# Kernel tuning notes

Measured on AMD Instinct MI355X. Metric: run time of the kernel, lower is better.

The kernel has to match this reference:

```python
import jax, jax.numpy as jnp
import numpy as np

B, N, D, H, DH, L, DFF, NSP = 2048, 64, 256, 8, 32, 3, 1024, 120
SCALE = 0.05


def _layernorm(x, g, b, eps=1e-5):
    m = x.mean(-1, keepdims=True)
    v = ((x - m) ** 2).mean(-1, keepdims=True)
    return (x - m) * jax.lax.rsqrt(v + eps) * g + b


def forward_core(input_messages, momenta, edge_vectors, edge_distances, cutoff_factors,
                 edge_w, edge_b, node_table, mom_w, mom_b, node_comp_w, node_comp_b,
                 nbr_table, comp_w1, comp_b1, comp_w2, comp_b2,
                 qkv_w, qkv_b, attn_out_w, attn_out_b, ln1_g, ln1_b,
                 ffn_w1, ffn_b1, ffn_w2, ffn_b2, ln2_g, ln2_b,
                 padding_mask, element_indices_nodes, element_indices_neighbors):
    silu = jax.nn.silu
    # NodeEncoder: element embedding + momenta projection, compressed to d_model
    node = node_table[element_indices_nodes]                       # [B, D]
    mom = momenta @ mom_w + mom_b                                  # [B, D]
    node = jnp.concatenate([node, mom], -1) @ node_comp_w + node_comp_b  # [B, D]
    # edge embedding: [vec(3), dist(1)] -> Linear(4, D)
    edge = jnp.concatenate([edge_vectors, edge_distances[..., None]], -1) @ edge_w + edge_b  # [B,N,D]
    # merge edge / neighbor-element / incoming message embeddings, compress MLP
    tok = jnp.concatenate([edge, nbr_table[element_indices_neighbors], input_messages], -1)  # [B,N,3D]
    tok = silu(tok @ comp_w1 + comp_b1) @ comp_w2 + comp_b2        # [B,N,D]
    x = jnp.concatenate([node[:, None, :], tok], 1)                # [B,S,D], S=N+1
    # cutoff factors: prepend 1 for central token, zero padded tokens, apply as log-bias over keys
    ones_col = jnp.ones((x.shape[0], 1), x.dtype)
    cf = jnp.concatenate([ones_col, cutoff_factors], 1)            # [B,S]
    mask = jnp.concatenate([jnp.ones((x.shape[0], 1), bool), padding_mask], 1)
    cf = jnp.where(mask, cf, jnp.zeros((), x.dtype))
    bias = jnp.where(cf > 0, jnp.log(jnp.maximum(cf, 1e-30)), jnp.full((), -1e9, x.dtype))
    bias = bias[:, None, None, :]                                  # [B,1,1,S] (key dim)
    Bsz, S, _ = x.shape
    inv_sqrt_dh = 1.0 / np.sqrt(DH).astype(np.float32)
    for l in range(L):  # PostLN transformer layers
        qkv = (x @ qkv_w[l] + qkv_b[l]).reshape(Bsz, S, 3, H, DH)
        q, k, v = qkv[:, :, 0], qkv[:, :, 1], qkv[:, :, 2]         # [B,S,H,DH]
        scores = jnp.einsum('bqhd,bkhd->bhqk', q, k) * inv_sqrt_dh + bias
        a = jax.nn.softmax(scores, axis=-1)                        # cutoff-modulated attention
        o = jnp.einsum('bhqk,bkhd->bqhd', a, v).reshape(Bsz, S, D)
        x = _layernorm(x + (o @ attn_out_w[l] + attn_out_b[l]), ln1_g[l], ln1_b[l])
        h = silu(x @ ffn_w1[l] + ffn_b1[l]) @ ffn_w2[l] + ffn_b2[l]
        x = _layernorm(x + h, ln2_g[l], ln2_b[l])
    return x


def setup_inputs() -> dict:
    key = jax.random.key(0)
    ks = iter(jax.random.split(key, 48))
    def nrm(shape, s=SCALE):
        return jax.random.normal(next(ks), shape, dtype=jnp.float32) * s
    inp = {
        'input_messages': jax.random.normal(next(ks), (B, N, D), dtype=jnp.float32),
        'momenta': jax.random.normal(next(ks), (B, 3), dtype=jnp.float32),
        'edge_vectors': jax.random.normal(next(ks), (B, N, 3), dtype=jnp.float32),
        'edge_distances': jax.random.uniform(next(ks), (B, N), dtype=jnp.float32) * 5.0,
        'cutoff_factors': jax.random.uniform(next(ks), (B, N), dtype=jnp.float32),
        'padding_mask': jnp.ones((B, N), dtype=bool),
        'element_indices_nodes': jax.random.randint(next(ks), (B,), 0, NSP),
        'element_indices_neighbors': jax.random.randint(next(ks), (B, N), 0, NSP),
        'edge_w': nrm((4, D)), 'edge_b': jnp.zeros((D,), jnp.float32),
        'node_table': nrm((NSP, D), 1.0), 'mom_w': nrm((3, D)), 'mom_b': jnp.zeros((D,), jnp.float32),
        'node_comp_w': nrm((2 * D, D)), 'node_comp_b': jnp.zeros((D,), jnp.float32),
        'nbr_table': nrm((NSP, D), 1.0),
        'comp_w1': nrm((3 * D, D)), 'comp_b1': jnp.zeros((D,), jnp.float32),
        'comp_w2': nrm((D, D)), 'comp_b2': jnp.zeros((D,), jnp.float32),
        'qkv_w': nrm((L, D, 3 * D)), 'qkv_b': jnp.zeros((L, 3 * D), jnp.float32),
        'attn_out_w': nrm((L, D, D)), 'attn_out_b': jnp.zeros((L, D), jnp.float32),
        'ln1_g': jnp.ones((L, D), jnp.float32), 'ln1_b': jnp.zeros((L, D), jnp.float32),
        'ffn_w1': nrm((L, D, DFF)), 'ffn_b1': jnp.zeros((L, DFF), jnp.float32),
        'ffn_w2': nrm((L, DFF, D)), 'ffn_b2': jnp.zeros((L, D), jnp.float32),
        'ln2_g': jnp.ones((L, D), jnp.float32), 'ln2_b': jnp.zeros((L, D), jnp.float32),
        'use_manual_attention': 1,
    }
    return inp


def reference(input_messages, momenta, edge_vectors, edge_distances, cutoff_factors,
              padding_mask, element_indices_nodes, element_indices_neighbors,
              edge_w, edge_b, node_table, mom_w, mom_b, node_comp_w, node_comp_b,
              nbr_table, comp_w1, comp_b1, comp_w2, comp_b2,
              qkv_w, qkv_b, attn_out_w, attn_out_b, ln1_g, ln1_b,
              ffn_w1, ffn_b1, ffn_w2, ffn_b2, ln2_g, ln2_b, use_manual_attention):
    # use_manual_attention selects an implementation path in torch; math is identical.
    x = forward_core(input_messages, momenta, edge_vectors, edge_distances, cutoff_factors,
                     edge_w, edge_b, node_table, mom_w, mom_b, node_comp_w, node_comp_b,
                     nbr_table, comp_w1, comp_b1, comp_w2, comp_b2,
                     qkv_w, qkv_b, attn_out_w, attn_out_b, ln1_g, ln1_b,
                     ffn_w1, ffn_b1, ffn_w2, ffn_b2, ln2_g, ln2_b,
                     padding_mask, element_indices_nodes, element_indices_neighbors)
    return x[:, 0, :], x[:, 1:, :]
```

## Files before the change

### kernel.cpp

```cpp
#include <hip/hip_runtime.h>
#include <hip/hip_bf16.h>

#define NT 512
typedef unsigned short u16;
typedef short s16x8 __attribute__((ext_vector_type(8)));
typedef float f32x4 __attribute__((ext_vector_type(4)));

constexpr int B_ = 2048, N_ = 64, S_ = 65, D_ = 256, L_ = 3;

constexpr size_t CW1T_OFF = 0;
constexpr size_t CW2T_OFF = 196608;
constexpr size_t QKVWT_OFF = 262144;
constexpr size_t AOWT_OFF = 851968;
constexpr size_t FW1T_OFF = 1048576;
constexpr size_t FW2T_OFF = 1835008;
constexpr size_t WS_W_BYTES = 5242880;
constexpr size_t X_OFF     = WS_W_BYTES;
constexpr size_t OSLOT_OFF = X_OFF + 68157440;
constexpr size_t BIG_OFF   = OSLOT_OFF + 68157440;
constexpr size_t WS_NEEDED = BIG_OFF + 272629760;

#define MFMA16(a, b, c) __builtin_amdgcn_mfma_f32_16x16x32_bf16(a, b, c, 0, 0, 0)

typedef __attribute__((address_space(3))) unsigned int lds_uint;
// ... 19 lines not shown
  for (int o = 32; o > 0; o >>= 1) v = fmaxf(v, __shfl_xor(v, o));
  return v;
}
__device__ __forceinline__ void unpack8(const u16* p, float* f) {
  uint4 u = *reinterpret_cast<const uint4*>(p);
  f[0] = __uint_as_float(u.x << 16); f[1] = __uint_as_float(u.x & 0xffff0000u);
  f[2] = __uint_as_float(u.y << 16); f[3] = __uint_as_float(u.y & 0xffff0000u);
  f[4] = __uint_as_float(u.z << 16); f[5] = __uint_as_float(u.z & 0xffff0000u);
  f[6] = __uint_as_float(u.w << 16); f[7] = __uint_as_float(u.w & 0xffff0000u);
}

__global__ void wconv(const float* __restrict__ src, u16* __restrict__ dst, int K, int N) {
  const size_t bo = (size_t)blockIdx.y * K * N;
  int idx = blockIdx.x * 256 + threadIdx.x;
  if (idx >= K * N) return;
  int n = idx / K, k = idx - n * K;
  dst[bo + idx] = f2b(src[bo + (size_t)k * N + n]);
}


template <int M, int N, int K, int EPI>
__global__ __launch_bounds__(512, 4) void gemm_bt(
    const u16* __restrict__ A, const u16* __restrict__ Bt,
    const float* __restrict__ bias, u16* __restrict__ C) {
  constexpr int MT_ = M / 128, NT_ = N / 256;
  constexpr int CHUNK = (MT_ * NT_) / 8;
  const int logical = (blockIdx.x % 8) * CHUNK + blockIdx.x / 8;
  const int mt = logical / NT_, nt = logical % NT_;
  const int m0 = mt * 128, n0 = nt * 256;
  const int tid = threadIdx.x, lane = tid & 63, w = tid >> 6;
  const int lr = lane & 15, lg = lane >> 4;
  const int wr = w >> 2, wc = w & 3;

  __shared__ __align__(16) u16 sm[64 * 264];
  u16* As = sm;
  u16* Bs = sm + 4096;
  f32x4 acc[4][4] = {};

  const int arow = w * 16 + (lane >> 2);
  const int brow = w * 32 + (lane >> 2);
  const int scol = (lane & 3) * 8;

  for (int k0 = 0; k0 < K; k0 += 32) {
    __syncthreads();
    gload_lds16(&A[(size_t)(m0 + arow) * K + k0 + scol],       &As[(w * 16) * 32]);
    gload_lds16(&Bt[(size_t)(n0 + brow) * K + k0 + scol],      &Bs[(w * 32) * 32]);
    gload_lds16(&Bt[(size_t)(n0 + brow + 16) * K + k0 + scol], &Bs[(w * 32 + 16) * 32]);
    __syncthreads();
    s16x8 af[4], bf[4];
#pragma unroll
    for (int i = 0; i < 4; ++i)
      af[i] = *(const s16x8*)&As[(wr * 64 + i * 16 + lr) * 32 + lg * 8];
#pragma unroll
    for (int j = 0; j < 4; ++j)
      bf[j] = *(const s16x8*)&Bs[(wc * 64 + j * 16 + lr) * 32 + lg * 8];
#pragma unroll
    for (int i = 0; i < 4; ++i)
#pragma unroll
      for (int j = 0; j < 4; ++j)
        acc[i][j] = MFMA16(af[i], bf[j], acc[i][j]);
  }

#pragma unroll
  for (int h = 0; h < 2; ++h) {
    __syncthreads();
    if (wr == h) {
#pragma unroll
      for (int j = 0; j < 4; ++j) {
        const int nl = wc * 64 + j * 16 + lr;
        const float bb = (EPI == 0) ? 0.0f : bias[n0 + nl];
#pragma unroll
        for (int i = 0; i < 4; ++i)
#pragma unroll
          for (int e = 0; e < 4; ++e) {
            float v = acc[i][j][e] + bb;
            if (EPI == 2) v = v * sigm(v);
            sm[(i * 16 + lg * 4 + e) * 264 + nl] = f2b(v);
          }
      }
    }
    __syncthreads();
    const int mbase = m0 + h * 64;
    const size_t gbase = (EPI == 3) ? (size_t)((mbase >> 6) * 65 + 1) : (size_t)mbase;
#pragma unroll
    for (int p = 0; p < 4; ++p) {
      int idx = tid + p * 512;
      int row = idx >> 5, c8 = idx & 31;
      *(uint4*)&C[(gbase + row) * N + n0 + c8 * 8] = *(const uint4*)&sm[row * 264 + c8 * 8];
    }
  }
}

__global__ __launch_bounds__(256) void resln(
    u16* __restrict__ x, const u16* __restrict__ delta,
    const float* __restrict__ cbias, const float* __restrict__ g,
    const float* __restrict__ bb) {
  const int lane = threadIdx.x & 63, w = threadIdx.x >> 6;
  const float4 gv = *(const float4*)&g[lane * 4];
  const float4 bv = *(const float4*)&bb[lane * 4];
  const float4 cb = *(const float4*)&cbias[lane * 4];
  for (int r = blockIdx.x * 4 + w; r < 133120; r += 8192) {
    uint2 xu = *(const uint2*)&x[(size_t)r * 256 + lane * 4];
    uint2 du = *(const uint2*)&delta[(size_t)r * 256 + lane * 4];
    float v0 = __uint_as_float(xu.x << 16) + __uint_as_float(du.x << 16) + cb.x;
    float v1 = __uint_as_float(xu.x & 0xffff0000u) + __uint_as_float(du.x & 0xffff0000u) + cb.y;
    float v2 = __uint_as_float(xu.y << 16) + __uint_as_float(du.y << 16) + cb.z;
    float v3 = __uint_as_float(xu.y & 0xffff0000u) + __uint_as_float(du.y & 0xffff0000u) + cb.w;
    float mean = wave_sum(v0 + v1 + v2 + v3) * (1.0f / 256.0f);
    float d0 = v0 - mean, d1 = v1 - mean, d2 = v2 - mean, d3 = v3 - mean;
    float var = wave_sum(d0 * d0 + d1 * d1 + d2 * d2 + d3 * d3) * (1.0f / 256.0f);
    float rs = rsqrtf(var + 1e-5f);
    uint2 p;
    p.x = f2b(d0 * rs * gv.x + bv.x) | ((unsigned)f2b(d1 * rs * gv.y + bv.y) << 16);
    p.y = f2b(d2 * rs * gv.z + bv.z) | ((unsigned)f2b(d3 * rs * gv.w + bv.w) << 16);
    *(uint2*)&x[(size_t)r * 256 + lane * 4] = p;
  }
}

__global__ __launch_bounds__(512) void embed_k(
    const float* __restrict__ msgs, const float* __restrict__ edge_vec,
    const float* __restrict__ edge_dist, const int* __restrict__ enb,
    const float* __restrict__ edge_w, const float* __restrict__ edge_b,
    const float* __restrict__ nbr_table, u16* __restrict__ T) {
  const int r0 = blockIdx.x * 64, tid = threadIdx.x;
  __shared__ float tv[64][4];
  if (tid < 256) {
    int r = tid >> 2, j = tid & 3;
    tv[r][j] = (j < 3) ? edge_vec[(size_t)(r0 + r) * 3 + j] : edge_dist[r0 + r];
  }
  __syncthreads();
  for (int idx = tid; idx < 64 * 192; idx += 512) {
    int r = idx / 192, c4 = (idx % 192) * 4;
    size_t gn = (size_t)r0 + r;
    float4 v;
    if (c4 < 256) {
      float t0 = tv[r][0], t1 = tv[r][1], t2 = tv[r][2], t3 = tv[r][3];
      const float4 w0 = *(const float4*)&edge_w[c4];
      const float4 w1 = *(const float4*)&edge_w[256 + c4];
      const float4 w2 = *(const float4*)&edge_w[512 + c4];
      const float4 w3 = *(const float4*)&edge_w[768 + c4];
      const float4 eb4 = *(const float4*)&edge_b[c4];
      v.x = t0 * w0.x + t1 * w1.x + t2 * w2.x + t3 * w3.x + eb4.x;
      v.y = t0 * w0.y + t1 * w1.y + t2 * w2.y + t3 * w3.y + eb4.y;
      v.z = t0 * w0.z + t1 * w1.z + t2 * w2.z + t3 * w3.z + eb4.z;
      v.w = t0 * w0.w + t1 * w1.w + t2 * w2.w + t3 * w3.w + eb4.w;
    } else if (c4 < 512) {
      v = *(const float4*)&nbr_table[(size_t)enb[gn] * 256 + (c4 - 256)];
    } else {
      v = *(const float4*)&msgs[gn * 256 + (c4 - 512)];
    }
    uint2 p;
    p.x = f2b(v.x) | ((unsigned)f2b(v.y) << 16);
    p.y = f2b(v.z) | ((unsigned)f2b(v.w) << 16);
    *(uint2*)&T[gn * 768 + c4] = p;
  }
}

__global__ __launch_bounds__(256) void node_row(
    const float* __restrict__ momenta, const int* __restrict__ ein,
    const float* __restrict__ node_table, const float* __restrict__ mom_w,
    const float* __restrict__ mom_b, const float* __restrict__ ncw,
    const float* __restrict__ ncb, u16* __restrict__ x) {
  const int b = blockIdx.x, tid = threadIdx.x;
  __shared__ float cvec[512];
  cvec[tid] = node_table[(size_t)ein[b] * 256 + tid];
  float m0 = momenta[b * 3], m1 = momenta[b * 3 + 1], m2 = momenta[b * 3 + 2];
  cvec[256 + tid] = m0 * mom_w[tid] + m1 * mom_w[256 + tid] + m2 * mom_w[512 + tid] + mom_b[tid];
  __syncthreads();
  float acc = 0.0f;
  for (int k = 0; k < 512; k += 4) {
    const float4 cv = *(const float4*)&cvec[k];
    acc += cv.x * ncw[(k + 0) * 256 + tid] + cv.y * ncw[(k + 1) * 256 + tid] +
// ... 55 lines not shown
  }
  __syncthreads();

  const int nt0 = wp ? 3 : 0, nt1 = wp ? 5 : 3;
  for (int nt = nt0; nt < nt1; ++nt) {
    s16x8 bq = *(const s16x8*)&Qs[hl][nt * 16 + lr][lg * 8];
    f32x4 sacc[5];
#pragma unroll
    for (int mt = 0; mt < 5; ++mt) {
      s16x8 ak = *(const s16x8*)&Ks[hl][mt * 16 + lr][lg * 8];
      f32x4 z = {0.f, 0.f, 0.f, 0.f};
      sacc[mt] = MFMA16(ak, bq, z);
    }
    float pv[5][4];
    float cmax = -3e38f;
#pragma unroll
    for (int mt = 0; mt < 5; ++mt)
#pragma unroll
      for (int e = 0; e < 4; ++e) {
        float v = sacc[mt][e] * 0.17677669529663687f + bias_s[mt * 16 + lg * 4 + e];
        pv[mt][e] = v;
        cmax = fmaxf(cmax, v);
      }
    cmax = fmaxf(cmax, __shfl_xor(cmax, 16));
    cmax = fmaxf(cmax, __shfl_xor(cmax, 32));
    float csum = 0.f;
#pragma unroll
    for (int mt = 0; mt < 5; ++mt)
#pragma unroll
      for (int e = 0; e < 4; ++e) {
        float p = __expf(pv[mt][e] - cmax);
        pv[mt][e] = p;
        csum += p;
      }
    csum += __shfl_xor(csum, 16);
    csum += __shfl_xor(csum, 32);
    float rinv = 1.0f / csum;
    const int q = nt * 16 + lr;
#pragma unroll
    for (int mt = 0; mt < 5; ++mt) {
      uint2 pk;
      pk.x = (unsigned)f2b(pv[mt][0] * rinv) | ((unsigned)f2b(pv[mt][1] * rinv) << 16);
      pk.y = (unsigned)f2b(pv[mt][2] * rinv) | ((unsigned)f2b(pv[mt][3] * rinv) << 16);
      *(uint2*)&Ps[hl][q][mt * 16 + lg * 4] = pk;
    }
  }
  __syncthreads();

  s16x8 vb[2][3];
#pragma unroll
  for (int d2 = 0; d2 < 2; ++d2)
#pragma unroll
    for (int ks = 0; ks < 3; ++ks)
      vb[d2][ks] = *(const s16x8*)&Vt[hl][d2 * 16 + lr][ks * 32 + lg * 8];
  const int mt0 = wp ? 3 : 0, mt1 = wp ? 5 : 3;
  for (int mt = mt0; mt < mt1; ++mt) {
    f32x4 oa[2] = {};
#pragma unroll
    for (int ks = 0; ks < 3; ++ks) {
      s16x8 pa = *(const s16x8*)&Ps[hl][mt * 16 + lr][ks * 32 + lg * 8];
#pragma unroll
      for (int d2 = 0; d2 < 2; ++d2) oa[d2] = MFMA16(pa, vb[d2][ks], oa[d2]);
    }
#pragma unroll
    for (int e = 0; e < 4; ++e) {
      int q = mt * 16 + lg * 4 + e;
      if (q < 65) {
        u16* op = o + (bs0 + q) * 256 + hp * 64 + hl * 32;
        op[lr] = f2b(oa[0][e]);
        op[16 + lr] = f2b(oa[1][e]);
      }
    }
  }
}

__global__ __launch_bounds__(256) void out_copy(const u16* __restrict__ x,
                                                float* __restrict__ out) {
  const int b = blockIdx.x, tid = threadIdx.x;
  out[(size_t)b * 256 + tid] = b2f(x[(size_t)b * 65 * 256 + tid]);
  float* out2 = out + (size_t)2048 * 256;
  for (int i = tid; i < 64 * 256; i += 256) {
    int s = i >> 8, c = i & 255;
    out2[((size_t)b * 64 + s) * 256 + c] = b2f(x[((size_t)b * 65 + 1 + s) * 256 + c]);
  }
}


__device__ __forceinline__ void lnorm(float (*xs)[D_], const float* g, const float* b,
                                      int wave, int lane) {
  for (int r = wave; r < S_; r += 8) {
    float v0 = xs[r][lane], v1 = xs[r][lane + 64], v2 = xs[r][lane + 128], v3 = xs[r][lane + 192];
    float mean = wave_sum(v0 + v1 + v2 + v3) * (1.0f / D_);
    float d0 = v0 - mean, d1 = v1 - mean, d2 = v2 - mean, d3 = v3 - mean;
    float var = wave_sum(d0 * d0 + d1 * d1 + d2 * d2 + d3 * d3) * (1.0f / D_);
    float rs = rsqrtf(var + 1e-5f);
    xs[r][lane]       = d0 * rs * g[lane]       + b[lane];
    xs[r][lane + 64]  = d1 * rs * g[lane + 64]  + b[lane + 64];
    xs[r][lane + 128] = d2 * rs * g[lane + 128] + b[lane + 128];
    xs[r][lane + 192] = d3 * rs * g[lane + 192] + b[lane + 192];
  }
}

__device__ __forceinline__ void stage_xb(const float (*xs)[D_], u16* xb, int tid) {
  for (int idx = tid; idx < S_ * 32; idx += NT) {
    int r = idx >> 5, c8 = (idx & 31) << 3;
    const float4 a = *(const float4*)&xs[r][c8];
    const float4 c = *(const float4*)&xs[r][c8 + 4];
    uint4 p;
    p.x = f2b(a.x) | ((unsigned)f2b(a.y) << 16);
    p.y = f2b(a.z) | ((unsigned)f2b(a.w) << 16);
    p.z = f2b(c.x) | ((unsigned)f2b(c.y) << 16);
    p.w = f2b(c.z) | ((unsigned)f2b(c.w) << 16);
    *reinterpret_cast<uint4*>(&xb[r * 264 + c8]) = p;
  }
}

__global__ __launch_bounds__(NT, 1) void cart_kernel(
    const float* __restrict__ msgs, const float* __restrict__ momenta,
    const float* __restrict__ edge_vec, const float* __restrict__ edge_dist,
    const float* __restrict__ cutoff, const int* __restrict__ ein,
    const int* __restrict__ enb, const float* __restrict__ edge_w,
    const float* __restrict__ edge_b, const float* __restrict__ node_table,
    const float* __restrict__ mom_w, const float* __restrict__ mom_b,
    const float* __restrict__ ncw, const float* __restrict__ ncb,
    const float* __restrict__ nbr_table, const float* __restrict__ cb1,
    const float* __restrict__ cb2, const float* __restrict__ qkv_b,
    const float* __restrict__ aob, const float* __restrict__ ln1g,
    const float* __restrict__ ln1b, const float* __restrict__ fb1,
    const float* __restrict__ fb2, const float* __restrict__ ln2g,
    const float* __restrict__ ln2b, const u16* __restrict__ cw1t,
    const u16* __restrict__ cw2t, const u16* __restrict__ qkvwt,
    const u16* __restrict__ aowt, const u16* __restrict__ fw1t,
    const u16* __restrict__ fw2t, float* __restrict__ out) {
  const int b = blockIdx.x, tid = threadIdx.x;
  const int lane = tid & 63, wave = tid >> 6;
  const int lr = lane & 15, lg = lane >> 4;

  __shared__ float xs[S_][D_];
  __shared__ __align__(16) u16 xb[80 * 264];
  __shared__ __align__(16) unsigned char pool[44928];
  __shared__ float bias_s[S_];

  u16* qkv2  = (u16*)pool;
  u16* och   = (u16*)(pool + 31200);
  float* arw = (float*)(pool + 42720);
  float* tvals = (float*)pool;
  float* cvec  = (float*)(pool + 1024);
  u16* h1s   = (u16*)pool;

  if (tid < S_) {
    if (tid == 0) bias_s[0] = 0.0f;
    else {
      float cf = cutoff[b * N_ + (tid - 1)];
      bias_s[tid] = (cf > 0.0f) ? logf(fmaxf(cf, 1e-30f)) : -1e9f;
    }
  }
  if (tid < 256) {
    int r = tid >> 2, j = tid & 3;
    tvals[tid] = (j < 3) ? edge_vec[(size_t)(b * N_ + r) * 3 + j] : edge_dist[b * N_ + r];
    cvec[tid] = node_table[(size_t)ein[b] * D_ + tid];
  } else {
    int t = tid - 256;
    float m0 = momenta[b * 3 + 0], m1 = momenta[b * 3 + 1], m2 = momenta[b * 3 + 2];
    cvec[256 + t] = m0 * mom_w[t] + m1 * mom_w[256 + t] + m2 * mom_w[512 + t] + mom_b[t];
  }
  __syncthreads();
  if (tid < 256) {
    float acc = 0.0f;
    for (int k = 0; k < 512; k += 4) {
      const float4 cv = *(const float4*)&cvec[k];
      acc += cv.x * ncw[(k + 0) * D_ + tid] + cv.y * ncw[(k + 1) * D_ + tid] +
             cv.z * ncw[(k + 2) * D_ + tid] + cv.w * ncw[(k + 3) * D_ + tid];
    }
    xs[0][tid] = acc + ncb[tid];
  }

  {
    f32x4 a1[2][4] = {};
    for (int ch = 0; ch < 3; ++ch) {
      __syncthreads();
      for (int idx = tid; idx < 64 * 64; idx += NT) {
        int r = idx >> 6, c4 = (idx & 63) << 2;
        int gn = b * N_ + r;
        float v0, v1, v2, v3;
        if (ch == 0) {
          float t0 = tvals[r * 4], t1 = tvals[r * 4 + 1], t2 = tvals[r * 4 + 2], t3 = tvals[r * 4 + 3];
          const float4 w0 = *(const float4*)&edge_w[c4];
          const float4 w1 = *(const float4*)&edge_w[256 + c4];
          const float4 w2 = *(const float4*)&edge_w[512 + c4];
          const float4 w3 = *(const float4*)&edge_w[768 + c4];
          const float4 bb = *(const float4*)&edge_b[c4];
          v0 = t0 * w0.x + t1 * w1.x + t2 * w2.x + t3 * w3.x + bb.x;
          v1 = t0 * w0.y + t1 * w1.y + t2 * w2.y + t3 * w3.y + bb.y;
          v2 = t0 * w0.z + t1 * w1.z + t2 * w2.z + t3 * w3.z + bb.z;
          v3 = t0 * w0.w + t1 * w1.w + t2 * w2.w + t3 * w3.w + bb.w;
        } else if (ch == 1) {
          const float4 v = *(const float4*)&nbr_table[(size_t)enb[gn] * D_ + c4];
          v0 = v.x; v1 = v.y; v2 = v.z; v3 = v.w;
        } else {
          const float4 v = *(const float4*)&msgs[(size_t)gn * D_ + c4];
          v0 = v.x; v1 = v.y; v2 = v.z; v3 = v.w;
        }
        uint2 p;
        p.x = f2b(v0) | ((unsigned)f2b(v1) << 16);
        p.y = f2b(v2) | ((unsigned)f2b(v3) << 16);
        *reinterpret_cast<uint2*>(&xb[r * 264 + c4]) = p;
      }
      __syncthreads();
#pragma unroll
      for (int ks = 0; ks < 8; ++ks) {
        s16x8 af[4];
#pragma unroll
        for (int mt = 0; mt < 4; ++mt)
          af[mt] = *(const s16x8*)&xb[(mt * 16 + lr) * 264 + ks * 32 + lg * 8];
#pragma unroll
        for (int ntl = 0; ntl < 2; ++ntl) {
          int nt = wave * 2 + ntl;
          s16x8 bf = *(const s16x8*)&cw1t[(size_t)(nt * 16 + lr) * 768 + ch * 256 + ks * 32 + lg * 8];
#pragma unroll
          for (int mt = 0; mt < 4; ++mt) a1[ntl][mt] = MFMA16(af[mt], bf, a1[ntl][mt]);
        }
      }
    }
    __syncthreads();
#pragma unroll
    for (int ntl = 0; ntl < 2; ++ntl) {
      int col = (wave * 2 + ntl) * 16 + lr;
      float bb = cb1[col];
#pragma unroll
      for (int mt = 0; mt < 4; ++mt)
#pragma unroll
        for (int e = 0; e < 4; ++e) {
          int r = mt * 16 + lg * 4 + e;
          float a = a1[ntl][mt][e] + bb;
          xb[r * 264 + col] = f2b(a * sigm(a));
        }
    }
    __syncthreads();
    f32x4 a2[2][4] = {};
#pragma unroll
    for (int ks = 0; ks < 8; ++ks) {
      s16x8 af[4];
#pragma unroll
      for (int mt = 0; mt < 4; ++mt)
        af[mt] = *(const s16x8*)&xb[(mt * 16 + lr) * 264 + ks * 32 + lg * 8];
#pragma unroll
      for (int ntl = 0; ntl < 2; ++ntl) {
        s16x8 bf = *(const s16x8*)&cw2t[(size_t)((wave * 2 + ntl) * 16 + lr) * 256 + ks * 32 + lg * 8];
#pragma unroll
        for (int mt = 0; mt < 4; ++mt) a2[ntl][mt] = MFMA16(af[mt], bf, a2[ntl][mt]);
      }
    }
#pragma unroll
    for (int ntl = 0; ntl < 2; ++ntl) {
      int col = (wave * 2 + ntl) * 16 + lr;
      float bb = cb2[col];
#pragma unroll
      for (int mt = 0; mt < 4; ++mt)
#pragma unroll
        for (int e = 0; e < 4; ++e) {
          int r = mt * 16 + lg * 4 + e;
          xs[1 + r][col] = a2[ntl][mt][e] + bb;
        }
    }
    __syncthreads();
  }

  for (int l = 0; l < L_; ++l) {
    stage_xb(xs, xb, tid);
    __syncthreads();
    f32x4 oacc[2][5] = {};
    const u16* Wq = qkvwt + (size_t)l * 768 * 256;
    const u16* Wo = aowt + (size_t)l * 256 * 256;
    for (int g = 0; g < 4; ++g) {
#pragma unroll
      for (int jj = 0; jj < 3; ++jj) {
        int j = wave * 3 + jj;
        int nt = j >> 1, half = j & 1;
        int m = nt >> 2, loc16 = (nt & 3) << 4;
        int nrow = m * 256 + g * 64 + loc16 + lr;
        int mt0 = half ? 3 : 0, nmt = half ? 2 : 3;
        f32x4 acc[3] = {};
#pragma unroll
        for (int ks = 0; ks < 8; ++ks) {
          s16x8 bf = *(const s16x8*)&Wq[(size_t)nrow * 256 + ks * 32 + lg * 8];
#pragma unroll
          for (int i = 0; i < 3; ++i)
            if (i < nmt) {
              s16x8 af = *(const s16x8*)&xb[((mt0 + i) * 16 + lr) * 264 + ks * 32 + lg * 8];
              acc[i] = MFMA16(af, bf, acc[i]);
            }
        }
        int colL = loc16 + lr;
        int hl = colL >> 5, d = colL & 31;
        float bb = qkv_b[l * 768 + nrow];
        u16* qdst = qkv2 + (size_t)(m * 2 + hl) * S_ * 40;
#pragma unroll
        for (int i = 0; i < 3; ++i)
          if (i < nmt)
#pragma unroll
            for (int e = 0; e < 4; ++e) {
              int r = (mt0 + i) * 16 + lg * 4 + e;
              if (r < S_) qdst[r * 40 + d] = f2b(acc[i][e] + bb);
            }
      }
      __syncthreads();
      for (int t = wave; t < 2 * S_; t += 8) {
        int hl = (t >= S_) ? 1 : 0;
        int q = t - hl * S_;
        const u16* qp = qkv2 + ((size_t)(0 + hl) * S_ + q) * 40;
        const u16* kp = qkv2 + (size_t)(2 + hl) * S_ * 40;
        const u16* vp = qkv2 + (size_t)(4 + hl) * S_ * 40;
        float sa = 0.0f, sb = 0.0f;
#pragma unroll
        for (int c8 = 0; c8 < 4; ++c8) {
          float qv[8], kl[8], k6[8];
          unpack8(qp + c8 * 8, qv);
          unpack8(kp + lane * 40 + c8 * 8, kl);
          unpack8(kp + 64 * 40 + c8 * 8, k6);
#pragma unroll
          for (int u = 0; u < 8; ++u) {
            sa = fmaf(qv[u], kl[u], sa);
            sb = fmaf(qv[u], k6[u], sb);
          }
        }
        sa = sa * 0.17677669529663687f + bias_s[lane];
        sb = sb * 0.17677669529663687f + bias_s[64];
        float mx = fmaxf(wave_max(sa), sb);
        float ea = __expf(sa - mx), eb = __expf(sb - mx);
        float denom = wave_sum(ea) + eb;
        float rinv = 1.0f / denom;
        arw[wave * 68 + lane] = ea;
        if (lane == 0) arw[wave * 68 + 64] = eb;
        int dd = lane & 31, hf = lane >> 5;
        float acc = 0.0f;
        for (int kk = hf; kk < S_; kk += 2)
          acc = fmaf(arw[wave * 68 + kk], b2f(vp[kk * 40 + dd]), acc);
        acc += __shfl_xor(acc, 32);
        if (lane < 32) och[q * 72 + hl * 32 + dd] = f2b(acc * rinv);
      }
      __syncthreads();
#pragma unroll
      for (int ks = 0; ks < 2; ++ks) {
        s16x8 af[5];
#pragma unroll
        for (int mt = 0; mt < 5; ++mt)
          af[mt] = *(const s16x8*)&och[(mt * 16 + lr) * 72 + ks * 32 + lg * 8];
#pragma unroll
        for (int ntl = 0; ntl < 2; ++ntl) {
          s16x8 bf = *(const s16x8*)&Wo[(size_t)((wave * 2 + ntl) * 16 + lr) * 256 + g * 64 + ks * 32 + lg * 8];
#pragma unroll
          for (int mt = 0; mt < 5; ++mt) oacc[ntl][mt] = MFMA16(af[mt], bf, oacc[ntl][mt]);
        }
      }
      __syncthreads();
    }
#pragma unroll
    for (int ntl = 0; ntl < 2; ++ntl) {
      int col = (wave * 2 + ntl) * 16 + lr;
      float bb = aob[l * 256 + col];
#pragma unroll
      for (int mt = 0; mt < 5; ++mt)
#pragma unroll
        for (int e = 0; e < 4; ++e) {
          int r = mt * 16 + lg * 4 + e;
          if (r < S_) xs[r][col] += oacc[ntl][mt][e] + bb;
        }
    }
    __syncthreads();
    lnorm(xs, ln1g + l * D_, ln1b + l * D_, wave, lane);
    __syncthreads();
    stage_xb(xs, xb, tid);
    __syncthreads();
    f32x4 facc[2][5] = {};
    const u16* W1 = fw1t + (size_t)l * 1024 * 256;
    const u16* W2 = fw2t + (size_t)l * 256 * 1024;
    for (int c = 0; c < 4; ++c) {
      f32x4 h1a[2][5] = {};
#pragma unroll
      for (int ks = 0; ks < 8; ++ks) {
        s16x8 af[5];
#pragma unroll
        for (int mt = 0; mt < 5; ++mt)
          af[mt] = *(const s16x8*)&xb[(mt * 16 + lr) * 264 + ks * 32 + lg * 8];
#pragma unroll
        for (int ntl = 0; ntl < 2; ++ntl) {
          s16x8 bf = *(const s16x8*)&W1[(size_t)(c * 256 + (wave * 2 + ntl) * 16 + lr) * 256 + ks * 32 + lg * 8];
#pragma unroll
          for (int mt = 0; mt < 5; ++mt) h1a[ntl][mt] = MFMA16(af[mt], bf, h1a[ntl][mt]);
        }
      }
#pragma unroll
      for (int ntl = 0; ntl < 2; ++ntl) {
        int colc = (wave * 2 + ntl) * 16 + lr;
        float bb = fb1[l * 1024 + c * 256 + colc];
#pragma unroll
        for (int mt = 0; mt < 5; ++mt)
#pragma unroll
          for (int e = 0; e < 4; ++e) {
            int r = mt * 16 + lg * 4 + e;
            float a = h1a[ntl][mt][e] + bb;
            h1s[r * 264 + colc] = f2b(a * sigm(a));
          }
      }
      __syncthreads();
#pragma unroll
      for (int ks = 0; ks < 8; ++ks) {
        s16x8 af[5];
#pragma unroll
        for (int mt = 0; mt < 5; ++mt)
          af[mt] = *(const s16x8*)&h1s[(mt * 16 + lr) * 264 + ks * 32 + lg * 8];
#pragma unroll
        for (int ntl = 0; ntl < 2; ++ntl) {
          s16x8 bf = *(const s16x8*)&W2[(size_t)((wave * 2 + ntl) * 16 + lr) * 1024 + c * 256 + ks * 32 + lg * 8];
#pragma unroll
          for (int mt = 0; mt < 5; ++mt) facc[ntl][mt] = MFMA16(af[mt], bf, facc[ntl][mt]);
        }
      }
      __syncthreads();
    }
#pragma unroll
    for (int ntl = 0; ntl < 2; ++ntl) {
      int col = (wave * 2 + ntl) * 16 + lr;
      float bb = fb2[l * 256 + col];
#pragma unroll
      for (int mt = 0; mt < 5; ++mt)
#pragma unroll
        for (int e = 0; e < 4; ++e) {
          int r = mt * 16 + lg * 4 + e;
          if (r < S_) xs[r][col] += facc[ntl][mt][e] + bb;
        }
    }
    __syncthreads();
    lnorm(xs, ln2g + l * D_, ln2b + l * D_, wave, lane);
    __syncthreads();
  }

  for (int idx = tid; idx < D_ / 4; idx += NT)
    ((float4*)out)[b * (D_ / 4) + idx] = *(const float4*)&xs[0][idx * 4];
  float4* out2 = (float4*)(out + (size_t)B_ * D_);
  for (int idx = tid; idx < N_ * D_ / 4; idx += NT) {
    int n = idx >> 6, c4 = idx & 63;
    out2[(size_t)(b * N_ + n) * 64 + c4] = *(const float4*)&xs[1 + n][c4 * 4];
  }
}


extern "C" void kernel_launch(void* const* d_in, const int* in_sizes, int n_in,
                              void* d_out, int out_size, void* d_ws, size_t ws_size,
                              hipStream_t stream) {
  (void)in_sizes; (void)n_in; (void)out_size;
  const float* msgs      = (const float*)d_in[0];
  const float* momenta   = (const float*)d_in[1];
  const float* edge_vec  = (const float*)d_in[2];
  const float* edge_dist = (const float*)d_in[3];
  const float* cutoff    = (const float*)d_in[4];
  const int* ein = (const int*)d_in[6];
  const int* enb = (const int*)d_in[7];
  const float* edge_w     = (const float*)d_in[8];
  const float* edge_b     = (const float*)d_in[9];
  const float* node_table = (const float*)d_in[10];
  const float* mom_w      = (const float*)d_in[11];
  const float* mom_b      = (const float*)d_in[12];
  const float* ncw        = (const float*)d_in[13];
  const float* ncb        = (const float*)d_in[14];
  const float* nbr_table  = (const float*)d_in[15];
  const float* cw1        = (const float*)d_in[16];
  const float* cb1        = (const float*)d_in[17];
  const float* cw2        = (const float*)d_in[18];
  const float* cb2        = (const float*)d_in[19];
  const float* qkv_w      = (const float*)d_in[20];
  const float* qkv_b      = (const float*)d_in[21];
  const float* aow        = (const float*)d_in[22];
  const float* aob        = (const float*)d_in[23];
  const float* ln1g       = (const float*)d_in[24];
  const float* ln1b       = (const float*)d_in[25];
  const float* fw1        = (const float*)d_in[26];
  const float* fb1        = (const float*)d_in[27];
  const float* fw2        = (const float*)d_in[28];
  const float* fb2        = (const float*)d_in[29];
  const float* ln2g       = (const float*)d_in[30];
  const float* ln2b       = (const float*)d_in[31];

  u16* ws = (u16*)d_ws;
  u16* cw1t  = ws + CW1T_OFF;
  u16* cw2t  = ws + CW2T_OFF;
  u16* qkvwt = ws + QKVWT_OFF;
  u16* aowt  = ws + AOWT_OFF;
  u16* fw1t  = ws + FW1T_OFF;
  u16* fw2t  = ws + FW2T_OFF;

  wconv<<<dim3((768 * 256 + 255) / 256, 1), 256, 0, stream>>>(cw1, cw1t, 768, 256);
  wconv<<<dim3((256 * 256 + 255) / 256, 1), 256, 0, stream>>>(cw2, cw2t, 256, 256);
  wconv<<<dim3((256 * 768 + 255) / 256, 3), 256, 0, stream>>>(qkv_w, qkvwt, 256, 768);
  wconv<<<dim3((256 * 256 + 255) / 256, 3), 256, 0, stream>>>(aow, aowt, 256, 256);
  wconv<<<dim3((256 * 1024 + 255) / 256, 3), 256, 0, stream>>>(fw1, fw1t, 256, 1024);
  wconv<<<dim3((1024 * 256 + 255) / 256, 3), 256, 0, stream>>>(fw2, fw2t, 1024, 256);

  if (ws_size >= WS_NEEDED) {
    u16* x    = (u16*)((char*)d_ws + X_OFF);
    u16* oslt = (u16*)((char*)d_ws + OSLOT_OFF);
    u16* big  = (u16*)((char*)d_ws + BIG_OFF);

    embed_k<<<2048, 512, 0, stream>>>(msgs, edge_vec, edge_dist, enb, edge_w,
                                      edge_b, nbr_table, big);
    gemm_bt<131072, 256, 768, 2><<<1024, 512, 0, stream>>>(big, cw1t, cb1, oslt);
    gemm_bt<131072, 256, 256, 3><<<1024, 512, 0, stream>>>(oslt, cw2t, cb2, x);
    node_row<<<2048, 256, 0, stream>>>(momenta, ein, node_table, mom_w, mom_b,
                                       ncw, ncb, x);
    for (int l = 0; l < 3; ++l) {
      gemm_bt<133120, 768, 256, 1><<<3120, 512, 0, stream>>>(
          x, qkvwt + (size_t)l * 196608, qkv_b + l * 768, big);
      attn_k2<<<dim3(2048, 4), 256, 0, stream>>>(big, cutoff, oslt);
      gemm_bt<133120, 256, 256, 0><<<1040, 512, 0, stream>>>(
          oslt, aowt + (size_t)l * 65536, aob, big);
      resln<<<2048, 256, 0, stream>>>(x, big, aob + l * 256, ln1g + l * 256,
                                      ln1b + l * 256);
      gemm_bt<133120, 1024, 256, 2><<<4160, 512, 0, stream>>>(
          x, fw1t + (size_t)l * 262144, fb1 + l * 1024, big);
      gemm_bt<133120, 256, 1024, 0><<<1040, 512, 0, stream>>>(
          big, fw2t + (size_t)l * 262144, fb2, oslt);
      resln<<<2048, 256, 0, stream>>>(x, oslt, fb2 + l * 256, ln2g + l * 256,
                                      ln2b + l * 256);
    }
    out_copy<<<2048, 256, 0, stream>>>(x, (float*)d_out);
  } else {
    cart_kernel<<<dim3(B_), dim3(NT), 0, stream>>>(
        msgs, momenta, edge_vec, edge_dist, cutoff, ein, enb, edge_w, edge_b,
        node_table, mom_w, mom_b, ncw, ncb, nbr_table, cb1, cb2, qkv_b, aob,
        ln1g, ln1b, fb1, fb2, ln2g, ln2b, cw1t, cw2t, qkvwt, aowt, fw1t, fw2t,
        (float*)d_out);
  }
}
```

Before: 2.082 ms.

## Fuse FFN up and down projections into one kernel keeping hidden tile in LDS

Adds an ffn_fused kernel that computes the FFN for a 64-row tile, holding the SiLU hidden activations in shared memory in 128-column chunks and accumulating the down projection in registers. This replaces the two separate gemm_bt launches, so the 133120x1024 bf16 hidden tensor is no longer written to and read back from global memory. It also removes the single-kernel cart_kernel fallback path. Each block now re-streams the full W1 and W2 weights through small LDS tiles with two barriers per 32-wide k step and no double buffering, so the matrix cores may stall more than in the tuned GEMM.

```diff
diff --git a/kernel.cpp b/kernel.cpp
--- a/kernel.cpp
+++ b/kernel.cpp
@@ -125,12 +125,113 @@
     __syncthreads();
     const int mbase = m0 + h * 64;
     const size_t gbase = (EPI == 3) ? (size_t)((mbase >> 6) * 65 + 1) : (size_t)mbase;
-#pragma unroll
-    for (int p = 0; p < 4; ++p) {
-      int idx = tid + p * 512;
+    for (int idx = tid; idx < 64 * 32; idx += 512) {
       int row = idx >> 5, c8 = idx & 31;
       *(uint4*)&C[(gbase + row) * N + n0 + c8 * 8] = *(const uint4*)&sm[row * 264 + c8 * 8];
     }
+  }
+}
+
+__global__ __launch_bounds__(256, 2) void ffn_fused(
+    const u16* __restrict__ x, const u16* __restrict__ W1t,
+    const float* __restrict__ b1, const u16* __restrict__ W2t,
+    u16* __restrict__ outd) {
+  constexpr int CHUNK_SW = 2080 / 8;
+  const int logical = (blockIdx.x % 8) * CHUNK_SW + blockIdx.x / 8;
+  const int m0 = logical * 64;
+  const int tid = threadIdx.x, lane = tid & 63, w = tid >> 6;
+  const int lr = lane & 15, lg = lane >> 4;
+  const int wr = w >> 1, wc = w & 1;
+  const int g_sub = lane >> 2, g_col = (lane & 3) * 8;
+
+  __shared__ __align__(16) u16 xs[64 * 264];
+  __shared__ __align__(16) u16 h1s[64 * 136];
+  __shared__ __align__(16) u16 Bs[256 * 32];
+
+  for (int idx = tid; idx < 64 * 32; idx += 256) {
+    int row = idx >> 5, c8 = idx & 31;
+    *(uint4*)&xs[row * 264 + c8 * 8] =
+        *(const uint4*)&x[(size_t)(m0 + row) * 256 + c8 * 8];
+  }
+
+  f32x4 aout[4][4] = {};
+
+  for (int c = 0; c < 8; ++c) {
+    f32x4 a1[2][4] = {};
+    for (int k0 = 0; k0 < 256; k0 += 32) {
+      __syncthreads();
+      gload_lds16(&W1t[(size_t)(c * 128 + w * 32 + g_sub) * 256 + k0 + g_col],
+                  &Bs[(w * 32) * 32]);
+      gload_lds16(&W1t[(size_t)(c * 128 + w * 32 + 16 + g_sub) * 256 + k0 + g_col],
+                  &Bs[(w * 32 + 16) * 32]);
+      __syncthreads();
+      s16x8 af[2], bf[4];
+#pragma unroll
+      for (int i = 0; i < 2; ++i)
+        af[i] = *(const s16x8*)&xs[(wr * 32 + i * 16 + lr) * 264 + k0 + lg * 8];
+#pragma unroll
+      for (int j = 0; j < 4; ++j)
+        bf[j] = *(const s16x8*)&Bs[(wc * 64 + j * 16 + lr) * 32 + lg * 8];
+#pragma unroll
+      for (int i = 0; i < 2; ++i)
+#pragma unroll
+        for (int j = 0; j < 4; ++j)
+          a1[i][j] = MFMA16(af[i], bf[j], a1[i][j]);
+    }
+#pragma unroll
+    for (int j = 0; j < 4; ++j) {
+      const int ncol = wc * 64 + j * 16 + lr;
+      const float bb = b1[c * 128 + ncol];
+#pragma unroll
+      for (int i = 0; i < 2; ++i)
+#pragma unroll
+        for (int e = 0; e < 4; ++e) {
+          const int row = wr * 32 + i * 16 + lg * 4 + e;
+          float v = a1[i][j][e] + bb;
+          h1s[row * 136 + ncol] = f2b(v * sigm(v));
+        }
+    }
+    for (int kk = 0; kk < 128; kk += 32) {
+      __syncthreads();
+      gload_lds16(&W2t[(size_t)(w * 64 + g_sub) * 1024 + c * 128 + kk + g_col],
+                  &Bs[(w * 64) * 32]);
+      gload_lds16(&W2t[(size_t)(w * 64 + 16 + g_sub) * 1024 + c * 128 + kk + g_col],
+                  &Bs[(w * 64 + 16) * 32]);
+      gload_lds16(&W2t[(size_t)(w * 64 + 32 + g_sub) * 1024 + c * 128 + kk + g_col],
+                  &Bs[(w * 64 + 32) * 32]);
+      gload_lds16(&W2t[(size_t)(w * 64 + 48 + g_sub) * 1024 + c * 128 + kk + g_col],
+                  &Bs[(w * 64 + 48) * 32]);
+      __syncthreads();
+      s16x8 af[4], bf[4];
+#pragma unroll
+      for (int i = 0; i < 4; ++i)
+        af[i] = *(const s16x8*)&h1s[(i * 16 + lr) * 136 + kk + lg * 8];
+#pragma unroll
+      for (int j = 0; j < 4; ++j)
+        bf[j] = *(const s16x8*)&Bs[(w * 64 + j * 16 + lr) * 32 + lg * 8];
+#pragma unroll
+      for (int i = 0; i < 4; ++i)
+#pragma unroll
+        for (int j = 0; j < 4; ++j)
+          aout[i][j] = MFMA16(af[i], bf[j], aout[i][j]);
+    }
+  }
+
+  __syncthreads();
+#pragma unroll
+  for (int j = 0; j < 4; ++j) {
+    const int ncol = w * 64 + j * 16 + lr;
+#pragma unroll
+    for (int i = 0; i < 4; ++i)
+#pragma unroll
+      for (int e = 0; e < 4; ++e)
+        xs[(i * 16 + lg * 4 + e) * 264 + ncol] = f2b(aout[i][j][e]);
+  }
+  __syncthreads();
+  for (int idx = tid; idx < 64 * 32; idx += 256) {
+    int row = idx >> 5, c8 = idx & 31;
+    *(uint4*)&outd[(size_t)(m0 + row) * 256 + c8 * 8] =
+        *(const uint4*)&xs[row * 264 + c8 * 8];
   }
 }
 
@@ -352,366 +453,6 @@
   for (int i = tid; i < 64 * 256; i += 256) {
     int s = i >> 8, c = i & 255;
     out2[((size_t)b * 64 + s) * 256 + c] = b2f(x[((size_t)b * 65 + 1 + s) * 256 + c]);
-  }
-}
-
-
-__device__ __forceinline__ void lnorm(float (*xs)[D_], const float* g, const float* b,
-                                      int wave, int lane) {
-  for (int r = wave; r < S_; r += 8) {
-    float v0 = xs[r][lane], v1 = xs[r][lane + 64], v2 = xs[r][lane + 128], v3 = xs[r][lane + 192];
-    float mean = wave_sum(v0 + v1 + v2 + v3) * (1.0f / D_);
-    float d0 = v0 - mean, d1 = v1 - mean, d2 = v2 - mean, d3 = v3 - mean;
-    float var = wave_sum(d0 * d0 + d1 * d1 + d2 * d2 + d3 * d3) * (1.0f / D_);
-    float rs = rsqrtf(var + 1e-5f);
-    xs[r][lane]       = d0 * rs * g[lane]       + b[lane];
-    xs[r][lane + 64]  = d1 * rs * g[lane + 64]  + b[lane + 64];
-    xs[r][lane + 128] = d2 * rs * g[lane + 128] + b[lane + 128];
-    xs[r][lane + 192] = d3 * rs * g[lane + 192] + b[lane + 192];
-  }
-}
-
-__device__ __forceinline__ void stage_xb(const float (*xs)[D_], u16* xb, int tid) {
-  for (int idx = tid; idx < S_ * 32; idx += NT) {
-    int r = idx >> 5, c8 = (idx & 31) << 3;
-    const float4 a = *(const float4*)&xs[r][c8];
-    const float4 c = *(const float4*)&xs[r][c8 + 4];
-    uint4 p;
-    p.x = f2b(a.x) | ((unsigned)f2b(a.y) << 16);
-    p.y = f2b(a.z) | ((unsigned)f2b(a.w) << 16);
-    p.z = f2b(c.x) | ((unsigned)f2b(c.y) << 16);
-    p.w = f2b(c.z) | ((unsigned)f2b(c.w) << 16);
-    *reinterpret_cast<uint4*>(&xb[r * 264 + c8]) = p;
-  }
-}
-
-__global__ __launch_bounds__(NT, 1) void cart_kernel(
-    const float* __restrict__ msgs, const float* __restrict__ momenta,
-    const float* __restrict__ edge_vec, const float* __restrict__ edge_dist,
-    const float* __restrict__ cutoff, const int* __restrict__ ein,
-    const int* __restrict__ enb, const float* __restrict__ edge_w,
-    const float* __restrict__ edge_b, const float* __restrict__ node_table,
-    const float* __restrict__ mom_w, const float* __restrict__ mom_b,
-    const float* __restrict__ ncw, const float* __restrict__ ncb,
-    const float* __restrict__ nbr_table, const float* __restrict__ cb1,
-    const float* __restrict__ cb2, const float* __restrict__ qkv_b,
-    const float* __restrict__ aob, const float* __restrict__ ln1g,
-    const float* __restrict__ ln1b, const float* __restrict__ fb1,
-    const float* __restrict__ fb2, const float* __restrict__ ln2g,
-    const float* __restrict__ ln2b, const u16* __restrict__ cw1t,
-    const u16* __restrict__ cw2t, const u16* __restrict__ qkvwt,
-    const u16* __restrict__ aowt, const u16* __restrict__ fw1t,
-    const u16* __restrict__ fw2t, float* __restrict__ out) {
-  const int b = blockIdx.x, tid = threadIdx.x;
-  const int lane = tid & 63, wave = tid >> 6;
-  const int lr = lane & 15, lg = lane >> 4;
-
-  __shared__ float xs[S_][D_];
-  __shared__ __align__(16) u16 xb[80 * 264];
-  __shared__ __align__(16) unsigned char pool[44928];
-  __shared__ float bias_s[S_];
-
-  u16* qkv2  = (u16*)pool;
-  u16* och   = (u16*)(pool + 31200);
-  float* arw = (float*)(pool + 42720);
-  float* tvals = (float*)pool;
-  float* cvec  = (float*)(pool + 1024);
-  u16* h1s   = (u16*)pool;
-
-  if (tid < S_) {
-    if (tid == 0) bias_s[0] = 0.0f;
-    else {
-      float cf = cutoff[b * N_ + (tid - 1)];
-      bias_s[tid] = (cf > 0.0f) ? logf(fmaxf(cf, 1e-30f)) : -1e9f;
-    }
-  }
-  if (tid < 256) {
-    int r = tid >> 2, j = tid & 3;
-    tvals[tid] = (j < 3) ? edge_vec[(size_t)(b * N_ + r) * 3 + j] : edge_dist[b * N_ + r];
-    cvec[tid] = node_table[(size_t)ein[b] * D_ + tid];
-  } else {
-    int t = tid - 256;
-    float m0 = momenta[b * 3 + 0], m1 = momenta[b * 3 + 1], m2 = momenta[b * 3 + 2];
-    cvec[256 + t] = m0 * mom_w[t] + m1 * mom_w[256 + t] + m2 * mom_w[512 + t] + mom_b[t];
-  }
-  __syncthreads();
-  if (tid < 256) {
-    float acc = 0.0f;
-    for (int k = 0; k < 512; k += 4) {
-      const float4 cv = *(const float4*)&cvec[k];
-      acc += cv.x * ncw[(k + 0) * D_ + tid] + cv.y * ncw[(k + 1) * D_ + tid] +
-             cv.z * ncw[(k + 2) * D_ + tid] + cv.w * ncw[(k + 3) * D_ + tid];
-    }
-    xs[0][tid] = acc + ncb[tid];
-  }
-
-  {
-    f32x4 a1[2][4] = {};
-    for (int ch = 0; ch < 3; ++ch) {
-      __syncthreads();
-      for (int idx = tid; idx < 64 * 64; idx += NT) {
-        int r = idx >> 6, c4 = (idx & 63) << 2;
-        int gn = b * N_ + r;
-        float v0, v1, v2, v3;
-        if (ch == 0) {
-          float t0 = tvals[r * 4], t1 = tvals[r * 4 + 1], t2 = tvals[r * 4 + 2], t3 = tvals[r * 4 + 3];
-          const float4 w0 = *(const float4*)&edge_w[c4];
-          const float4 w1 = *(const float4*)&edge_w[256 + c4];
-          const float4 w2 = *(const float4*)&edge_w[512 + c4];
-          const float4 w3 = *(const float4*)&edge_w[768 + c4];
-          const float4 bb = *(const float4*)&edge_b[c4];
-          v0 = t0 * w0.x + t1 * w1.x + t2 * w2.x + t3 * w3.x + bb.x;
-          v1 = t0 * w0.y + t1 * w1.y + t2 * w2.y + t3 * w3.y + bb.y;
-          v2 = t0 * w0.z + t1 * w1.z + t2 * w2.z + t3 * w3.z + bb.z;
-          v3 = t0 * w0.w + t1 * w1.w + t2 * w2.w + t3 * w3.w + bb.w;
-        } else if (ch == 1) {
-          const float4 v = *(const float4*)&nbr_table[(size_t)enb[gn] * D_ + c4];
-          v0 = v.x; v1 = v.y; v2 = v.z; v3 = v.w;
-        } else {
-          const float4 v = *(const float4*)&msgs[(size_t)gn * D_ + c4];
-          v0 = v.x; v1 = v.y; v2 = v.z; v3 = v.w;
-        }
-        uint2 p;
-        p.x = f2b(v0) | ((unsigned)f2b(v1) << 16);
-        p.y = f2b(v2) | ((unsigned)f2b(v3) << 16);
-        *reinterpret_cast<uint2*>(&xb[r * 264 + c4]) = p;
-      }
-      __syncthreads();
-#pragma unroll
-      for (int ks = 0; ks < 8; ++ks) {
-        s16x8 af[4];
-#pragma unroll
-        for (int mt = 0; mt < 4; ++mt)
-          af[mt] = *(const s16x8*)&xb[(mt * 16 + lr) * 264 + ks * 32 + lg * 8];
-#pragma unroll
-        for (int ntl = 0; ntl < 2; ++ntl) {
-          int nt = wave * 2 + ntl;
-          s16x8 bf = *(const s16x8*)&cw1t[(size_t)(nt * 16 + lr) * 768 + ch * 256 + ks * 32 + lg * 8];
-#pragma unroll
-          for (int mt = 0; mt < 4; ++mt) a1[ntl][mt] = MFMA16(af[mt], bf, a1[ntl][mt]);
-        }
-      }
-    }
-    __syncthreads();
-#pragma unroll
-    for (int ntl = 0; ntl < 2; ++ntl) {
-      int col = (wave * 2 + ntl) * 16 + lr;
-      float bb = cb1[col];
-#pragma unroll
-      for (int mt = 0; mt < 4; ++mt)
-#pragma unroll
-        for (int e = 0; e < 4; ++e) {
-          int r = mt * 16 + lg * 4 + e;
-          float a = a1[ntl][mt][e] + bb;
-          xb[r * 264 + col] = f2b(a * sigm(a));
-        }
-    }
-    __syncthreads();
-    f32x4 a2[2][4] = {};
-#pragma unroll
-    for (int ks = 0; ks < 8; ++ks) {
-      s16x8 af[4];
-#pragma unroll
-      for (int mt = 0; mt < 4; ++mt)
-        af[mt] = *(const s16x8*)&xb[(mt * 16 + lr) * 264 + ks * 32 + lg * 8];
-#pragma unroll
-      for (int ntl = 0; ntl < 2; ++ntl) {
-        s16x8 bf = *(const s16x8*)&cw2t[(size_t)((wave * 2 + ntl) * 16 + lr) * 256 + ks * 32 + lg * 8];
-#pragma unroll
-        for (int mt = 0; mt < 4; ++mt) a2[ntl][mt] = MFMA16(af[mt], bf, a2[ntl][mt]);
-      }
-    }
-#pragma unroll
-    for (int ntl = 0; ntl < 2; ++ntl) {
-      int col = (wave * 2 + ntl) * 16 + lr;
-      float bb = cb2[col];
-#pragma unroll
-      for (int mt = 0; mt < 4; ++mt)
-#pragma unroll
-        for (int e = 0; e < 4; ++e) {
-          int r = mt * 16 + lg * 4 + e;
-          xs[1 + r][col] = a2[ntl][mt][e] + bb;
-        }
-    }
-    __syncthreads();
-  }
-
-  for (int l = 0; l < L_; ++l) {
-    stage_xb(xs, xb, tid);
-    __syncthreads();
-    f32x4 oacc[2][5] = {};
-    const u16* Wq = qkvwt + (size_t)l * 768 * 256;
-    const u16* Wo = aowt + (size_t)l * 256 * 256;
-    for (int g = 0; g < 4; ++g) {
-#pragma unroll
-      for (int jj = 0; jj < 3; ++jj) {
-        int j = wave * 3 + jj;
-        int nt = j >> 1, half = j & 1;
-        int m = nt >> 2, loc16 = (nt & 3) << 4;
-        int nrow = m * 256 + g * 64 + loc16 + lr;
-        int mt0 = half ? 3 : 0, nmt = half ? 2 : 3;
-        f32x4 acc[3] = {};
-#pragma unroll
-        for (int ks = 0; ks < 8; ++ks) {
-          s16x8 bf = *(const s16x8*)&Wq[(size_t)nrow * 256 + ks * 32 + lg * 8];
-#pragma unroll
-          for (int i = 0; i < 3; ++i)
-            if (i < nmt) {
-              s16x8 af = *(const s16x8*)&xb[((mt0 + i) * 16 + lr) * 264 + ks * 32 + lg * 8];
-              acc[i] = MFMA16(af, bf, acc[i]);
-            }
-        }
-        int colL = loc16 + lr;
-        int hl = colL >> 5, d = colL & 31;
-        float bb = qkv_b[l * 768 + nrow];
-        u16* qdst = qkv2 + (size_t)(m * 2 + hl) * S_ * 40;
-#pragma unroll
-        for (int i = 0; i < 3; ++i)
-          if (i < nmt)
-#pragma unroll
-            for (int e = 0; e < 4; ++e) {
-              int r = (mt0 + i) * 16 + lg * 4 + e;
-              if (r < S_) qdst[r * 40 + d] = f2b(acc[i][e] + bb);
-            }
-      }
-      __syncthreads();
-      for (int t = wave; t < 2 * S_; t += 8) {
-        int hl = (t >= S_) ? 1 : 0;
-        int q = t - hl * S_;
-        const u16* qp = qkv2 + ((size_t)(0 + hl) * S_ + q) * 40;
-        const u16* kp = qkv2 + (size_t)(2 + hl) * S_ * 40;
-        const u16* vp = qkv2 + (size_t)(4 + hl) * S_ * 40;
-        float sa = 0.0f, sb = 0.0f;
-#pragma unroll
-        for (int c8 = 0; c8 < 4; ++c8) {
-          float qv[8], kl[8], k6[8];
-          unpack8(qp + c8 * 8, qv);
-          unpack8(kp + lane * 40 + c8 * 8, kl);
-          unpack8(kp + 64 * 40 + c8 * 8, k6);
-#pragma unroll
-          for (int u = 0; u < 8; ++u) {
-            sa = fmaf(qv[u], kl[u], sa);
-            sb = fmaf(qv[u], k6[u], sb);
-          }
-        }
-        sa = sa * 0.17677669529663687f + bias_s[lane];
-        sb = sb * 0.17677669529663687f + bias_s[64];
-        float mx = fmaxf(wave_max(sa), sb);
-        float ea = __expf(sa - mx), eb = __expf(sb - mx);
-        float denom = wave_sum(ea) + eb;
-        float rinv = 1.0f / denom;
-        arw[wave * 68 + lane] = ea;
-        if (lane == 0) arw[wave * 68 + 64] = eb;
-        int dd = lane & 31, hf = lane >> 5;
-        float acc = 0.0f;
-        for (int kk = hf; kk < S_; kk += 2)
-          acc = fmaf(arw[wave * 68 + kk], b2f(vp[kk * 40 + dd]), acc);
-        acc += __shfl_xor(acc, 32);
-        if (lane < 32) och[q * 72 + hl * 32 + dd] = f2b(acc * rinv);
-      }
-      __syncthreads();
-#pragma unroll
-      for (int ks = 0; ks < 2; ++ks) {
-        s16x8 af[5];
-#pragma unroll
-        for (int mt = 0; mt < 5; ++mt)
-          af[mt] = *(const s16x8*)&och[(mt * 16 + lr) * 72 + ks * 32 + lg * 8];
-#pragma unroll
-        for (int ntl = 0; ntl < 2; ++ntl) {
-          s16x8 bf = *(const s16x8*)&Wo[(size_t)((wave * 2 + ntl) * 16 + lr) * 256 + g * 64 + ks * 32 + lg * 8];
-#pragma unroll
-          for (int mt = 0; mt < 5; ++mt) oacc[ntl][mt] = MFMA16(af[mt], bf, oacc[ntl][mt]);
-        }
-      }
-      __syncthreads();
-    }
-#pragma unroll
-    for (int ntl = 0; ntl < 2; ++ntl) {
-      int col = (wave * 2 + ntl) * 16 + lr;
-      float bb = aob[l * 256 + col];
-#pragma unroll
-      for (int mt = 0; mt < 5; ++mt)
-#pragma unroll
-        for (int e = 0; e < 4; ++e) {
-          int r = mt * 16 + lg * 4 + e;
-          if (r < S_) xs[r][col] += oacc[ntl][mt][e] + bb;
-        }
-    }
-    __syncthreads();
-    lnorm(xs, ln1g + l * D_, ln1b + l * D_, wave, lane);
-    __syncthreads();
-    stage_xb(xs, xb, tid);
-    __syncthreads();
-    f32x4 facc[2][5] = {};
-    const u16* W1 = fw1t + (size_t)l * 1024 * 256;
-    const u16* W2 = fw2t + (size_t)l * 256 * 1024;
-    for (int c = 0; c < 4; ++c) {
-      f32x4 h1a[2][5] = {};
-#pragma unroll
-      for (int ks = 0; ks < 8; ++ks) {
-        s16x8 af[5];
-#pragma unroll
-        for (int mt = 0; mt < 5; ++mt)
-          af[mt] = *(const s16x8*)&xb[(mt * 16 + lr) * 264 + ks * 32 + lg * 8];
-#pragma unroll
-        for (int ntl = 0; ntl < 2; ++ntl) {
-          s16x8 bf = *(const s16x8*)&W1[(size_t)(c * 256 + (wave * 2 + ntl) * 16 + lr) * 256 + ks * 32 + lg * 8];
-#pragma unroll
-          for (int mt = 0; mt < 5; ++mt) h1a[ntl][mt] = MFMA16(af[mt], bf, h1a[ntl][mt]);
-        }
-      }
-#pragma unroll
-      for (int ntl = 0; ntl < 2; ++ntl) {
-        int colc = (wave * 2 + ntl) * 16 + lr;
-        float bb = fb1[l * 1024 + c * 256 + colc];
-#pragma unroll
-        for (int mt = 0; mt < 5; ++mt)
-#pragma unroll
-          for (int e = 0; e < 4; ++e) {
-            int r = mt * 16 + lg * 4 + e;
-            float a = h1a[ntl][mt][e] + bb;
-            h1s[r * 264 + colc] = f2b(a * sigm(a));
-          }
-      }
-      __syncthreads();
-#pragma unroll
-      for (int ks = 0; ks < 8; ++ks) {
-        s16x8 af[5];
-#pragma unroll
-        for (int mt = 0; mt < 5; ++mt)
-          af[mt] = *(const s16x8*)&h1s[(mt * 16 + lr) * 264 + ks * 32 + lg * 8];
-#pragma unroll
-        for (int ntl = 0; ntl < 2; ++ntl) {
-          s16x8 bf = *(const s16x8*)&W2[(size_t)((wave * 2 + ntl) * 16 + lr) * 1024 + c * 256 + ks * 32 + lg * 8];
-#pragma unroll
-          for (int mt = 0; mt < 5; ++mt) facc[ntl][mt] = MFMA16(af[mt], bf, facc[ntl][mt]);
-        }
-      }
-      __syncthreads();
-    }
-#pragma unroll
-    for (int ntl = 0; ntl < 2; ++ntl) {
-      int col = (wave * 2 + ntl) * 16 + lr;
-      float bb = fb2[l * 256 + col];
-#pragma unroll
-      for (int mt = 0; mt < 5; ++mt)
-#pragma unroll
-        for (int e = 0; e < 4; ++e) {
-          int r = mt * 16 + lg * 4 + e;
-          if (r < S_) xs[r][col] += facc[ntl][mt][e] + bb;
-        }
-    }
-    __syncthreads();
-    lnorm(xs, ln2g + l * D_, ln2b + l * D_, wave, lane);
-    __syncthreads();
-  }
-
-  for (int idx = tid; idx < D_ / 4; idx += NT)
-    ((float4*)out)[b * (D_ / 4) + idx] = *(const float4*)&xs[0][idx * 4];
-  float4* out2 = (float4*)(out + (size_t)B_ * D_);
-  for (int idx = tid; idx < N_ * D_ / 4; idx += NT) {
-    int n = idx >> 6, c4 = idx & 63;
-    out2[(size_t)(b * N_ + n) * 64 + c4] = *(const float4*)&xs[1 + n][c4 * 4];
   }
 }
 
@@ -767,38 +508,29 @@
   wconv<<<dim3((256 * 1024 + 255) / 256, 3), 256, 0, stream>>>(fw1, fw1t, 256, 1024);
   wconv<<<dim3((1024 * 256 + 255) / 256, 3), 256, 0, stream>>>(fw2, fw2t, 1024, 256);
 
-  if (ws_size >= WS_NEEDED) {
-    u16* x    = (u16*)((char*)d_ws + X_OFF);
-    u16* oslt = (u16*)((char*)d_ws + OSLOT_OFF);
-    u16* big  = (u16*)((char*)d_ws + BIG_OFF);
-
-    embed_k<<<2048, 512, 0, stream>>>(msgs, edge_vec, edge_dist, enb, edge_w,
-                                      edge_b, nbr_table, big);
-    gemm_bt<131072, 256, 768, 2><<<1024, 512, 0, stream>>>(big, cw1t, cb1, oslt);
-    gemm_bt<131072, 256, 256, 3><<<1024, 512, 0, stream>>>(oslt, cw2t, cb2, x);
-    node_row<<<2048, 256, 0, stream>>>(momenta, ein, node_table, mom_w, mom_b,
-                                       ncw, ncb, x);
-    for (int l = 0; l < 3; ++l) {
-      gemm_bt<133120, 768, 256, 1><<<3120, 512, 0, stream>>>(
-          x, qkvwt + (size_t)l * 196608, qkv_b + l * 768, big);
-      attn_k2<<<dim3(2048, 4), 256, 0, stream>>>(big, cutoff, oslt);
-      gemm_bt<133120, 256, 256, 0><<<1040, 512, 0, stream>>>(
-          oslt, aowt + (size_t)l * 65536, aob, big);
-      resln<<<2048, 256, 0, stream>>>(x, big, aob + l * 256, ln1g + l * 256,
-                                      ln1b + l * 256);
-      gemm_bt<133120, 1024, 256, 2><<<4160, 512, 0, stream>>>(
-          x, fw1t + (size_t)l * 262144, fb1 + l * 1024, big);
-      gemm_bt<133120, 256, 1024, 0><<<1040, 512, 0, stream>>>(
-          big, fw2t + (size_t)l * 262144, fb2, oslt);
-      resln<<<2048, 256, 0, stream>>>(x, oslt, fb2 + l * 256, ln2g + l * 256,
-                                      ln2b + l * 256);
-    }
-    out_copy<<<2048, 256, 0, stream>>>(x, (float*)d_out);
-  } else {
-    cart_kernel<<<dim3(B_), dim3(NT), 0, stream>>>(
-        msgs, momenta, edge_vec, edge_dist, cutoff, ein, enb, edge_w, edge_b,
-        node_table, mom_w, mom_b, ncw, ncb, nbr_table, cb1, cb2, qkv_b, aob,
-        ln1g, ln1b, fb1, fb2, ln2g, ln2b, cw1t, cw2t, qkvwt, aowt, fw1t, fw2t,
-        (float*)d_out);
-  }
-}
+  u16* x    = (u16*)((char*)d_ws + X_OFF);
+  u16* oslt = (u16*)((char*)d_ws + OSLOT_OFF);
+  u16* big  = (u16*)((char*)d_ws + BIG_OFF);
+
+  embed_k<<<2048, 512, 0, stream>>>(msgs, edge_vec, edge_dist, enb, edge_w,
+                                    edge_b, nbr_table, big);
+  gemm_bt<131072, 256, 768, 2><<<1024, 512, 0, stream>>>(big, cw1t, cb1, oslt);
+  gemm_bt<131072, 256, 256, 3><<<1024, 512, 0, stream>>>(oslt, cw2t, cb2, x);
+  node_row<<<2048, 256, 0, stream>>>(momenta, ein, node_table, mom_w, mom_b,
+                                     ncw, ncb, x);
+  for (int l = 0; l < 3; ++l) {
+    gemm_bt<133120, 768, 256, 1><<<3120, 512, 0, stream>>>(
+        x, qkvwt + (size_t)l * 196608, qkv_b + l * 768, big);
+    attn_k2<<<dim3(2048, 4), 256, 0, stream>>>(big, cutoff, oslt);
+    gemm_bt<133120, 256, 256, 0><<<1040, 512, 0, stream>>>(
+        oslt, aowt + (size_t)l * 65536, aob, big);
+    resln<<<2048, 256, 0, stream>>>(x, big, aob + l * 256, ln1g + l * 256,
+                                    ln1b + l * 256);
+    ffn_fused<<<2080, 256, 0, stream>>>(
+        x, fw1t + (size_t)l * 262144, fb1 + l * 1024,
+        fw2t + (size_t)l * 262144, oslt);
+    resln<<<2048, 256, 0, stream>>>(x, oslt, fb2 + l * 256, ln2g + l * 256,
+                                    ln2b + l * 256);
+  }
+  out_copy<<<2048, 256, 0, stream>>>(x, (float*)d_out);
+}
```

New measurement: 2.239 ms. 1.08x slower.
